# Kernel tuning notes

Measured on AMD Instinct MI355X. Metric: run time of the kernel, lower is better.

The kernel has to match this reference:

```python
import jax, jax.numpy as jnp
import numpy as np

N_QUBITS = 6
N_LAYERS = 3
FEATURE_DIM = 512
ENC_HIDDEN = max(32, N_QUBITS * 4)  # 32
HEAD_HIDDEN = 128
G, T = 54, 24
DIM = 2 ** N_QUBITS  # 64


def _ry_batched(angles):
    # angles: [B] -> batched RY matrices [B, 2, 2] (complex64)
    c = jnp.cos(angles * 0.5)
    s = jnp.sin(angles * 0.5)
    U = jnp.stack([jnp.stack([c, -s], -1), jnp.stack([s, c], -1)], -2)
    return U.astype(jnp.complex64)


def _rot(phi, theta, omega):
    # PennyLane Rot = RZ(omega) RY(theta) RZ(phi); returns [2, 2] complex64
    c = jnp.cos(theta * 0.5).astype(jnp.complex64)
    s = jnp.sin(theta * 0.5).astype(jnp.complex64)
    ep = jnp.exp(-0.5j * (phi + omega).astype(jnp.complex64))  # e^{-i(phi+omega)/2}
    em = jnp.exp(-0.5j * (phi - omega).astype(jnp.complex64))  # e^{-i(phi-omega)/2}
    u00 = ep * c
    u01 = -jnp.conj(em) * s
    u10 = em * s
    u11 = jnp.conj(ep) * c
    return jnp.stack([jnp.stack([u00, u01]), jnp.stack([u10, u11])])


def _apply_1q_batched(state, U, q):
    # state: [B, 2^n]; U: [B, 2, 2] (per-sample gate, e.g. data-encoding RY)
    B = state.shape[0]
    st = state.reshape(B, 2 ** q, 2, -1)
    st = jnp.einsum('bij,bljr->blir', U, st)
    return st.reshape(B, -1)


def _apply_1q(state, U, q):
    # state: [B, 2^n]; U: [2, 2] shared across batch (trainable Rot)
    B = state.shape[0]
    st = state.reshape(B, 2 ** q, 2, -1)
    st = jnp.einsum('ij,bljr->blir', U, st)
    return st.reshape(B, -1)


def _apply_cnot(state, c, t):
    # state: [B, 2^n]; flip target axis where control bit == 1
    B = state.shape[0]
    st = state.reshape((B,) + (2,) * N_QUBITS)
    ax_c, ax_t = 1 + c, 1 + t
    s0 = jnp.take(st, 0, axis=ax_c)
    s1 = jnp.take(st, 1, axis=ax_c)
    s1 = jnp.flip(s1, axis=ax_t if ax_t < ax_c else ax_t - 1)
    st = jnp.stack([s0, s1], axis=ax_c)
    return st.reshape(B, -1)


def _expvals_z(state):
    # <Z_q> for every qubit: [B, n]
    B = state.shape[0]
    probs = (state.real ** 2 + state.imag ** 2).reshape((B,) + (2,) * N_QUBITS)
    outs = []
    for q in range(N_QUBITS):
        axes = tuple(i for i in range(1, N_QUBITS + 1) if i != q + 1)
        p = probs.sum(axes)  # [B, 2]
        outs.append(p[:, 0] - p[:, 1])
    return jnp.stack(outs, -1)


def _circuit(angles, q_weights):
    # angles: [B, n_qubits] float32; q_weights: [L, n, 3]
    B = angles.shape[0]
    state = jnp.zeros((B, DIM), jnp.complex64).at[:, 0].set(1.0)
    for layer in range(N_LAYERS):
        # data_reuploading=True -> re-encode every layer
        for q in range(N_QUBITS):
            state = _apply_1q_batched(state, _ry_batched(angles[:, q]), q)
        for q in range(N_QUBITS):
            w = q_weights[layer, q]
            state = _apply_1q(state, _rot(w[0], w[1], w[2]), q)
        for q in range(0, N_QUBITS - 1, 2):
            state = _apply_cnot(state, q, q + 1)
        for q in range(1, N_QUBITS - 1, 2):
            state = _apply_cnot(state, q, q + 1)
        state = _apply_cnot(state, N_QUBITS - 1, 0)  # n_qubits > 2
    return _expvals_z(state)


def setup_inputs() -> dict:
    key = jax.random.key(0)
    ks = jax.random.split(key, 10)
    B = 32768
    return {
        'x': jax.random.normal(ks[0], (B, FEATURE_DIM), jnp.float32),
        'enc_w1': 0.05 * jax.random.normal(ks[1], (FEATURE_DIM, ENC_HIDDEN), jnp.float32),
        'enc_b1': jnp.zeros((ENC_HIDDEN,), jnp.float32),
        'enc_w2': 0.05 * jax.random.normal(ks[2], (ENC_HIDDEN, N_QUBITS), jnp.float32),
        'enc_b2': jnp.zeros((N_QUBITS,), jnp.float32),
        'q_weights': 0.01 * jax.random.normal(ks[3], (N_LAYERS, N_QUBITS, 3), jnp.float32),
        'head_w1': 0.1 * jax.random.normal(ks[4], (N_QUBITS, HEAD_HIDDEN), jnp.float32),
        'head_b1': jnp.zeros((HEAD_HIDDEN,), jnp.float32),
        'head_w2': 0.05 * jax.random.normal(ks[5], (HEAD_HIDDEN, G * T), jnp.float32),
        'head_b2': jnp.zeros((G * T,), jnp.float32),
    }


def reference(x, enc_w1, enc_b1, enc_w2, enc_b2, q_weights,
              head_w1, head_b1, head_w2, head_b2):
    # classical encoder -> angles [B, n_qubits]
    h = jnp.tanh(x @ enc_w1 + enc_b1)
    angles = h @ enc_w2 + enc_b2
    # batched state-vector PQC simulation
    z = _circuit(angles, q_weights).astype(jnp.float32)  # [B, n_qubits]
    # classical head (dropout is identity in eval)
    g = jax.nn.relu(z @ head_w1 + head_b1)
    logits = g @ head_w2 + head_b2
    return logits.reshape(-1, G, T)
```

## Files before the change

### kernel.cpp

```cpp
#include <hip/hip_runtime.h>

typedef __bf16 bf16x8 __attribute__((ext_vector_type(8)));
typedef float floatx4 __attribute__((ext_vector_type(4)));
typedef unsigned short ushort8 __attribute__((ext_vector_type(8)));

__device__ __forceinline__ unsigned short f2bf(float f) {
    unsigned u = __float_as_uint(f);
    u += 0x7fffu + ((u >> 16) & 1u);
    return (unsigned short)(u >> 16);
}

template <int ST>
__device__ __forceinline__ void apply_local(float* fr, float* fi,
    float m00r, float m00i, float m01r, float m01i,
    float m10r, float m10i, float m11r, float m11i) {
#pragma unroll
    for (int i = 0; i < 8; ++i) {
        if ((i & ST) == 0) {
            int i1 = i + ST;
            float r0 = fr[i], u0 = fi[i], r1 = fr[i1], u1 = fi[i1];
            fr[i]  = m00r * r0 - m00i * u0 + m01r * r1 - m01i * u1;
            fi[i]  = m00r * u0 + m00i * r0 + m01r * u1 + m01i * r1;
            fr[i1] = m10r * r0 - m10i * u0 + m11r * r1 - m11i * u1;
            fi[i1] = m10r * u0 + m10i * r0 + m11r * u1 + m11i * r1;
        }
    }
}

template <int XM>
__device__ __forceinline__ void apply_cross(float* fr, float* fi, bool hi,
    float m00r, float m00i, float m01r, float m01i,
    float m10r, float m10i, float m11r, float m11i) {
    float car = hi ? m10r : m00r, cai = hi ? m10i : m00i;
    float cbr = hi ? m11r : m01r, cbi = hi ? m11i : m01i;
#pragma unroll
    for (int j = 0; j < 8; ++j) {
        float mr = fr[j], mi = fi[j];
        float pr = __shfl_xor(mr, XM);
        float pi = __shfl_xor(mi, XM);
        float a0r = hi ? pr : mr, a0i = hi ? pi : mi;
        float a1r = hi ? mr : pr, a1i = hi ? mi : pi;
        fr[j] = car * a0r - cai * a0i + cbr * a1r - cbi * a1i;
        fi[j] = car * a0i + cai * a0r + cbr * a1i + cbi * a1r;
    }
}

#define SWAP2(a, b) { float _t = fr[a]; fr[a] = fr[b]; fr[b] = _t; \
                      _t = fi[a]; fi[a] = fi[b]; fi[b] = _t; }

__global__ __launch_bounds__(512, 4) void fused_front(
    const float* __restrict__ x, const float* __restrict__ w1,
    const float* __restrict__ b1, const float* __restrict__ w2,
    const float* __restrict__ b2, const float* __restrict__ qw,
    const float* __restrict__ hw1, const float* __restrict__ hb1,
    const float* __restrict__ hw2,
    unsigned short* __restrict__ w2t, unsigned short* __restrict__ g) {

    if (blockIdx.x >= 512) {
        int t = (blockIdx.x - 512) * 512 + threadIdx.x;
        int nn = t >> 4;
        int kc = (t & 15) * 8;
        if (nn < 1296) {
            ushort8 pk;
#pragma unroll
            for (int j = 0; j < 8; ++j) pk[j] = f2bf(hw2[(size_t)(kc + j) * 1296 + nn]);
            *(ushort8*)(w2t + (size_t)nn * 128 + kc) = pk;
        }
        return;
    }

    __shared__ float part[8][64][33];
    __shared__ float umat_s[144];

    float (*hsh)[33] = part[0];
    float (*casa)[12] = (float (*)[12])part[1];
    float (*zsh)[6]   = (float (*)[6])part[2];

    int tid = threadIdx.x;

    if (tid < 18) {
        float phi = qw[tid * 3], theta = qw[tid * 3 + 1], omega = qw[tid * 3 + 2];
        float c = cosf(0.5f * theta), s = sinf(0.5f * theta);
        float po = 0.5f * (phi + omega), pm = 0.5f * (phi - omega);
        float epr = cosf(po), epi = -sinf(po);
        float emr = cosf(pm), emi = -sinf(pm);
        float* u = umat_s + tid * 8;
        u[0] = epr * c;  u[1] = epi * c;
        u[2] = -emr * s; u[3] = emi * s;
        u[4] = emr * s;  u[5] = emi * s;
        u[6] = epr * c;  u[7] = -epi * c;
    }

    int lane = tid & 63;
    int wave = tid >> 6;
    int swave = __builtin_amdgcn_readfirstlane(wave);
    size_t row = (size_t)blockIdx.x * 64 + lane;
    const float2* x2 = (const float2*)(x + row * 512 + swave * 64);
    const float* wseg = w1 + swave * 64 * 32;

    float acc[32];
#pragma unroll
    for (int j = 0; j < 32; ++j) acc[j] = 0.f;

#pragma clang loop unroll(disable)
    for (int k2 = 0; k2 < 32; ++k2) {
        float2 xv = x2[k2];
        const float* wr = wseg + k2 * 64;
#pragma unroll
        for (int j = 0; j < 32; ++j) acc[j] = fmaf(wr[j], xv.x, acc[j]);
#pragma unroll
        for (int j = 0; j < 32; ++j) acc[j] = fmaf(wr[32 + j], xv.y, acc[j]);
    }
#pragma unroll
    for (int j = 0; j < 32; ++j) part[wave][lane][j] = acc[j];
    __syncthreads();

    {
        int rl = tid & 63;
        int jg = (tid >> 6) * 4;
#pragma unroll
        for (int jj = 0; jj < 4; ++jj) {
            int j = jg + jj;
            float v = b1[j];
#pragma unroll
            for (int w = 0; w < 8; ++w) v += part[w][rl][j];
            hsh[rl][j] = tanhf(v);
        }
    }
    __syncthreads();

    if (tid < 384) {
        int row_a = tid & 63;
        int q = tid >> 6;
        float a = b2[q];
#pragma unroll
        for (int j = 0; j < 32; ++j) a = fmaf(hsh[row_a][j], w2[j * 6 + q], a);
        a *= 0.5f;
        casa[row_a][q * 2]     = cosf(a);
        casa[row_a][q * 2 + 1] = sinf(a);
    }
    __syncthreads();

    int s8 = lane & 7;
    int p = lane >> 3;
    int samp = wave * 8 + s8;
    bool pb4 = (p & 4) != 0, pb2 = (p & 2) != 0, pb1 = (p & 1) != 0;

    float ca[6], sa[6];
#pragma unroll
    for (int q = 0; q < 6; ++q) { ca[q] = casa[samp][q * 2]; sa[q] = casa[samp][q * 2 + 1]; }

    float fr[8], fi[8];
#pragma unroll
    for (int j = 0; j < 8; ++j) { fr[j] = 0.f; fi[j] = 0.f; }
    fr[0] = (p == 0) ? 1.f : 0.f;

#pragma clang loop unroll(disable)
    for (int layer = 0; layer < 3; ++layer) {
        const float* ub = umat_s + layer * 48;
#define MAT(Q)                                                            \
        const float* u = ub + (Q) * 8;                                    \
        float c = ca[Q], ss = sa[Q];                                      \
        float m00r = u[0] * c + u[2] * ss, m00i = u[1] * c + u[3] * ss;   \
        float m01r = u[2] * c - u[0] * ss, m01i = u[3] * c - u[1] * ss;   \
        float m10r = u[4] * c + u[6] * ss, m10i = u[5] * c + u[7] * ss;   \
        float m11r = u[6] * c - u[4] * ss, m11i = u[7] * c - u[5] * ss;
        { MAT(0) apply_cross<32>(fr, fi, pb4, m00r, m00i, m01r, m01i, m10r, m10i, m11r, m11i); }
        { MAT(1) apply_cross<16>(fr, fi, pb2, m00r, m00i, m01r, m01i, m10r, m10i, m11r, m11i); }
        { MAT(2) apply_cross<8>(fr, fi, pb1, m00r, m00i, m01r, m01i, m10r, m10i, m11r, m11i); }
        { MAT(3) apply_local<4>(fr, fi, m00r, m00i, m01r, m01i, m10r, m10i, m11r, m11i); }
        { MAT(4) apply_local<2>(fr, fi, m00r, m00i, m01r, m01i, m10r, m10i, m11r, m11i); }
        { MAT(5) apply_local<1>(fr, fi, m00r, m00i, m01r, m01i, m10r, m10i, m11r, m11i); }
#undef MAT
#pragma unroll
        for (int j = 0; j < 8; ++j) {
            float pr = __shfl_xor(fr[j], 16);
            float pi = __shfl_xor(fi[j], 16);
            fr[j] = pb4 ? pr : fr[j];
            fi[j] = pb4 ? pi : fi[j];
        }
        {
            float tr[8], ti[8];
#pragma unroll
            for (int j = 0; j < 8; ++j) { tr[j] = fr[j]; ti[j] = fi[j]; }
#pragma unroll
            for (int j = 0; j < 8; ++j) {
                fr[j] = pb1 ? tr[j ^ 4] : tr[j];
                fi[j] = pb1 ? ti[j ^ 4] : ti[j];
            }
        }
        SWAP2(2, 3) SWAP2(6, 7)
#pragma unroll
        for (int j = 0; j < 8; ++j) {
            float pr = __shfl_xor(fr[j], 8);
            float pi = __shfl_xor(fi[j], 8);
            fr[j] = pb2 ? pr : fr[j];
            fi[j] = pb2 ? pi : fi[j];
        }
        SWAP2(4, 6) SWAP2(5, 7)
#pragma unroll
        for (int j = 1; j < 8; j += 2) {
            fr[j] = __shfl_xor(fr[j], 32);
            fi[j] = __shfl_xor(fi[j], 32);
        }
    }

    float zt = 0.f, z3 = 0.f, z4 = 0.f, z5 = 0.f;
#pragma unroll
    for (int j = 0; j < 8; ++j) {
        float pp = fr[j] * fr[j] + fi[j] * fi[j];
        zt += pp;
        z3 += (j & 4) ? -pp : pp;
        z4 += (j & 2) ? -pp : pp;
        z5 += (j & 1) ? -pp : pp;
    }
    float zz[6];
    zz[0] = pb4 ? -zt : zt;
    zz[1] = pb2 ? -zt : zt;
    zz[2] = pb1 ? -zt : zt;
    zz[3] = z3; zz[4] = z4; zz[5] = z5;
#pragma unroll
    for (int q = 0; q < 6; ++q) {
        zz[q] += __shfl_xor(zz[q], 8);
        zz[q] += __shfl_xor(zz[q], 16);
        zz[q] += __shfl_xor(zz[q], 32);
    }
    if (p < 6) zsh[samp][p] = zz[p];
    __syncthreads();

    int samp_h = wave * 8 + (lane >> 3);
    int seg = lane & 7;
    float z6[6];
#pragma unroll
    for (int q = 0; q < 6; ++q) z6[q] = zsh[samp_h][q];
    size_t sglob = (size_t)blockIdx.x * 64 + samp_h;
    unsigned short* gp = g + sglob * 128 + seg * 16;
#pragma unroll
    for (int j0 = 0; j0 < 16; j0 += 8) {
        ushort8 pk;
#pragma unroll
        for (int jj = 0; jj < 8; ++jj) {
            int j = seg * 16 + j0 + jj;
            float a = hb1[j];
#pragma unroll
            for (int q = 0; q < 6; ++q) a = fmaf(z6[q], hw1[q * 128 + j], a);
            a = fmaxf(a, 0.f);
            pk[jj] = f2bf(a);
        }
        *(ushort8*)(gp + j0) = pk;
    }
}

__global__ __launch_bounds__(256) void head_gemm(
    const unsigned short* __restrict__ g, const unsigned short* __restrict__ w2t,
    const float* __restrict__ b2, float* __restrict__ out) {
    int lane = threadIdx.x & 63;
    int wv = threadIdx.x >> 6;
    int row0 = blockIdx.x * 32;
    int l15 = lane & 15, quad = lane >> 4;

    const unsigned short* bp = g + (size_t)(row0 + l15) * 128 + quad * 8;
    bf16x8 bfr[2][4];
#pragma unroll
    for (int sub = 0; sub < 2; ++sub)
#pragma unroll
        for (int ks = 0; ks < 4; ++ks)
            bfr[sub][ks] = *(const bf16x8*)(bp + (size_t)sub * 16 * 128 + ks * 32);

    for (int n = wv; n < 27; n += 4) {
        int col0 = n * 48;
        const unsigned short* ap = w2t + (size_t)(col0 + l15) * 128 + quad * 8;

        floatx4 acc[6];
#pragma unroll
        for (int i = 0; i < 6; ++i) acc[i] = (floatx4)0.f;

#pragma unroll
        for (int ks = 0; ks < 4; ++ks) {
            bf16x8 af[3];
#pragma unroll
            for (int t = 0; t < 3; ++t) af[t] = *(const bf16x8*)(ap + (size_t)t * 16 * 128 + ks * 32);
#pragma unroll
            for (int t = 0; t < 3; ++t)
#pragma unroll
                for (int sub = 0; sub < 2; ++sub)
                    acc[t * 2 + sub] = __builtin_amdgcn_mfma_f32_16x16x32_bf16(af[t], bfr[sub][ks], acc[t * 2 + sub], 0, 0, 0);
        }

#pragma unroll
        for (int t = 0; t < 3; ++t) {
            const float* bb = b2 + col0 + t * 16 + quad * 4;
            floatx4 bias = { bb[0], bb[1], bb[2], bb[3] };
#pragma unroll
            for (int sub = 0; sub < 2; ++sub) {
                floatx4 v = acc[t * 2 + sub] + bias;
                floatx4* dst = (floatx4*)(out + (size_t)(row0 + sub * 16 + l15) * 1296 + col0 + t * 16 + quad * 4);
                *dst = v;
            }
        }
    }
}

extern "C" void kernel_launch(void* const* d_in, const int* in_sizes, int n_in,
                              void* d_out, int out_size, void* d_ws, size_t ws_size,
                              hipStream_t stream) {
    const float* x   = (const float*)d_in[0];
    const float* ew1 = (const float*)d_in[1];
    const float* eb1 = (const float*)d_in[2];
    const float* ew2 = (const float*)d_in[3];
    const float* eb2 = (const float*)d_in[4];
    const float* qw  = (const float*)d_in[5];
    const float* hw1 = (const float*)d_in[6];
    const float* hb1 = (const float*)d_in[7];
    const float* hw2 = (const float*)d_in[8];
    const float* hb2 = (const float*)d_in[9];
    float* out = (float*)d_out;

    char* ws = (char*)d_ws;
    unsigned short* g   = (unsigned short*)(ws);
    unsigned short* w2t = (unsigned short*)(ws + 8388608);

    fused_front<<<dim3(553), dim3(512), 0, stream>>>(x, ew1, eb1, ew2, eb2, qw, hw1, hb1, hw2, w2t, g);
    head_gemm<<<dim3(1024), dim3(256), 0, stream>>>(g, w2t, hb2, out);
}
```

Before: 346.8 us.

## Fuse head GEMM into front kernel via swizzled shared-memory activations

The head GEMM moves into the front kernel. Each block now keeps its 64 samples' bf16 hidden activations in XOR-swizzled shared memory and runs the MFMA GEMM for those rows directly, instead of writing g to global memory and reading it back in a separate kernel. The weight transpose/convert to bf16 is split out into its own small prep kernel launched first. This removes the global round-trip of g and one kernel boundary. In exchange, the GEMM grid shrinks to 512 blocks of 8 waves each covering 27 column tiles, which gives uneven work per wave and more accumulator registers under the 4-blocks occupancy bound.

```diff
diff --git a/kernel.cpp b/kernel.cpp
--- a/kernel.cpp
+++ b/kernel.cpp
@@ -48,34 +48,33 @@
 #define SWAP2(a, b) { float _t = fr[a]; fr[a] = fr[b]; fr[b] = _t; \
                       _t = fi[a]; fi[a] = fi[b]; fi[b] = _t; }
 
-__global__ __launch_bounds__(512, 4) void fused_front(
+__global__ __launch_bounds__(512) void prep_kernel(
+    const float* __restrict__ hw2, unsigned short* __restrict__ w2t) {
+    int t = blockIdx.x * 512 + threadIdx.x;
+    int nn = t >> 4;
+    int kc = (t & 15) * 8;
+    if (nn < 1296) {
+        ushort8 pk;
+#pragma unroll
+        for (int j = 0; j < 8; ++j) pk[j] = f2bf(hw2[(size_t)(kc + j) * 1296 + nn]);
+        *(ushort8*)(w2t + (size_t)nn * 128 + kc) = pk;
+    }
+}
+
+__global__ __launch_bounds__(512, 4) void mega_kernel(
     const float* __restrict__ x, const float* __restrict__ w1,
     const float* __restrict__ b1, const float* __restrict__ w2,
     const float* __restrict__ b2, const float* __restrict__ qw,
     const float* __restrict__ hw1, const float* __restrict__ hb1,
-    const float* __restrict__ hw2,
-    unsigned short* __restrict__ w2t, unsigned short* __restrict__ g) {
-
-    if (blockIdx.x >= 512) {
-        int t = (blockIdx.x - 512) * 512 + threadIdx.x;
-        int nn = t >> 4;
-        int kc = (t & 15) * 8;
-        if (nn < 1296) {
-            ushort8 pk;
-#pragma unroll
-            for (int j = 0; j < 8; ++j) pk[j] = f2bf(hw2[(size_t)(kc + j) * 1296 + nn]);
-            *(ushort8*)(w2t + (size_t)nn * 128 + kc) = pk;
-        }
-        return;
-    }
+    const unsigned short* __restrict__ w2t, const float* __restrict__ hb2,
+    float* __restrict__ out) {
 
     __shared__ float part[8][64][33];
     __shared__ float umat_s[144];
 
     float (*hsh)[33] = part[0];
     float (*casa)[12] = (float (*)[12])part[1];
-    float (*zsh)[6]   = (float (*)[6])part[2];
-
+    char* gl = (char*)&part[3][0][0];
     int tid = threadIdx.x;
 
     if (tid < 18) {
@@ -225,77 +224,71 @@
         zz[q] += __shfl_xor(zz[q], 16);
         zz[q] += __shfl_xor(zz[q], 32);
     }
-    if (p < 6) zsh[samp][p] = zz[p];
+
+    {
+        int a7 = samp & 7;
+#pragma unroll
+        for (int half = 0; half < 2; ++half) {
+            ushort8 pk;
+#pragma unroll
+            for (int jj = 0; jj < 8; ++jj) {
+                int j = p * 16 + half * 8 + jj;
+                float a = hb1[j];
+#pragma unroll
+                for (int q = 0; q < 6; ++q) a = fmaf(zz[q], hw1[q * 128 + j], a);
+                a = fmaxf(a, 0.f);
+                pk[jj] = f2bf(a);
+            }
+            int u = (p * 2 + half) ^ a7;
+            *(ushort8*)(gl + samp * 256 + u * 16) = pk;
+        }
+    }
     __syncthreads();
 
-    int samp_h = wave * 8 + (lane >> 3);
-    int seg = lane & 7;
-    float z6[6];
-#pragma unroll
-    for (int q = 0; q < 6; ++q) z6[q] = zsh[samp_h][q];
-    size_t sglob = (size_t)blockIdx.x * 64 + samp_h;
-    unsigned short* gp = g + sglob * 128 + seg * 16;
-#pragma unroll
-    for (int j0 = 0; j0 < 16; j0 += 8) {
-        ushort8 pk;
-#pragma unroll
-        for (int jj = 0; jj < 8; ++jj) {
-            int j = seg * 16 + j0 + jj;
-            float a = hb1[j];
-#pragma unroll
-            for (int q = 0; q < 6; ++q) a = fmaf(z6[q], hw1[q * 128 + j], a);
-            a = fmaxf(a, 0.f);
-            pk[jj] = f2bf(a);
-        }
-        *(ushort8*)(gp + j0) = pk;
-    }
-}
-
-__global__ __launch_bounds__(256) void head_gemm(
-    const unsigned short* __restrict__ g, const unsigned short* __restrict__ w2t,
-    const float* __restrict__ b2, float* __restrict__ out) {
-    int lane = threadIdx.x & 63;
-    int wv = threadIdx.x >> 6;
-    int row0 = blockIdx.x * 32;
-    int l15 = lane & 15, quad = lane >> 4;
-
-    const unsigned short* bp = g + (size_t)(row0 + l15) * 128 + quad * 8;
-    bf16x8 bfr[2][4];
-#pragma unroll
-    for (int sub = 0; sub < 2; ++sub)
-#pragma unroll
-        for (int ks = 0; ks < 4; ++ks)
-            bfr[sub][ks] = *(const bf16x8*)(bp + (size_t)sub * 16 * 128 + ks * 32);
-
-    for (int n = wv; n < 27; n += 4) {
-        int col0 = n * 48;
-        const unsigned short* ap = w2t + (size_t)(col0 + l15) * 128 + quad * 8;
-
-        floatx4 acc[6];
-#pragma unroll
-        for (int i = 0; i < 6; ++i) acc[i] = (floatx4)0.f;
-
-#pragma unroll
-        for (int ks = 0; ks < 4; ++ks) {
-            bf16x8 af[3];
-#pragma unroll
-            for (int t = 0; t < 3; ++t) af[t] = *(const bf16x8*)(ap + (size_t)t * 16 * 128 + ks * 32);
-#pragma unroll
-            for (int t = 0; t < 3; ++t)
-#pragma unroll
-                for (int sub = 0; sub < 2; ++sub)
-                    acc[t * 2 + sub] = __builtin_amdgcn_mfma_f32_16x16x32_bf16(af[t], bfr[sub][ks], acc[t * 2 + sub], 0, 0, 0);
-        }
-
-#pragma unroll
-        for (int t = 0; t < 3; ++t) {
-            const float* bb = b2 + col0 + t * 16 + quad * 4;
-            floatx4 bias = { bb[0], bb[1], bb[2], bb[3] };
-#pragma unroll
-            for (int sub = 0; sub < 2; ++sub) {
-                floatx4 v = acc[t * 2 + sub] + bias;
-                floatx4* dst = (floatx4*)(out + (size_t)(row0 + sub * 16 + l15) * 1296 + col0 + t * 16 + quad * 4);
-                *dst = v;
+    {
+        int l15 = lane & 15, quad = lane >> 4;
+        int row0 = blockIdx.x * 64;
+        int a7 = l15 & 7;
+
+        for (int n = wave; n < 27; n += 8) {
+            int col0 = n * 48;
+            const unsigned short* ap = w2t + (size_t)(col0 + l15) * 128 + quad * 8;
+
+            floatx4 acc[12];
+#pragma unroll
+            for (int i = 0; i < 12; ++i) acc[i] = (floatx4)0.f;
+
+#pragma unroll
+            for (int ks = 0; ks < 4; ++ks) {
+                bf16x8 af[3], bf[4];
+#pragma unroll
+                for (int t = 0; t < 3; ++t)
+                    af[t] = *(const bf16x8*)(ap + (size_t)t * 16 * 128 + ks * 32);
+#pragma unroll
+                for (int sub = 0; sub < 4; ++sub) {
+                    int rowg = sub * 16 + l15;
+                    int u = (quad + 4 * ks) ^ a7;
+                    bf[sub] = *(const bf16x8*)(gl + rowg * 256 + u * 16);
+                }
+#pragma unroll
+                for (int t = 0; t < 3; ++t)
+#pragma unroll
+                    for (int sub = 0; sub < 4; ++sub)
+                        acc[t * 4 + sub] = __builtin_amdgcn_mfma_f32_16x16x32_bf16(
+                            af[t], bf[sub], acc[t * 4 + sub], 0, 0, 0);
+            }
+
+#pragma unroll
+            for (int t = 0; t < 3; ++t) {
+                const float* bb = hb2 + col0 + t * 16 + quad * 4;
+                floatx4 bias = { bb[0], bb[1], bb[2], bb[3] };
+#pragma unroll
+                for (int sub = 0; sub < 4; ++sub) {
+                    floatx4 v = acc[t * 4 + sub] + bias;
+                    floatx4* dst = (floatx4*)(out +
+                        (size_t)(row0 + sub * 16 + l15) * 1296 + col0 + t * 16 + quad * 4);
+                    *dst = v;
+                }
             }
         }
     }
@@ -317,9 +310,9 @@
     float* out = (float*)d_out;
 
     char* ws = (char*)d_ws;
-    unsigned short* g   = (unsigned short*)(ws);
-    unsigned short* w2t = (unsigned short*)(ws + 8388608);
-
-    fused_front<<<dim3(553), dim3(512), 0, stream>>>(x, ew1, eb1, ew2, eb2, qw, hw1, hb1, hw2, w2t, g);
-    head_gemm<<<dim3(1024), dim3(256), 0, stream>>>(g, w2t, hb2, out);
-}
+    unsigned short* w2t = (unsigned short*)(ws);
+
+    prep_kernel<<<dim3(41), dim3(512), 0, stream>>>(hw2, w2t);
+    mega_kernel<<<dim3(512), dim3(512), 0, stream>>>(
+        x, ew1, eb1, ew2, eb2, qw, hw1, hb1, w2t, hb2, out);
+}
```

Result: no change. 341.0 us (-1.7%).
